# Performance work log

Hardware: AMD Instinct MI355X
Metric: run time of the kernel (lower is better)

Reference implementation:

```python
import jax, jax.numpy as jnp
import numpy as np

GRID_RES = 128
SCALE = 2.0
DEFORM_SCALE = 1.0
N_VERTS = 200_000
N_TETS = 1_000_000

TRI_TABLE = np.array([
    [-1,-1,-1,-1,-1,-1],[1,0,2,-1,-1,-1],[4,0,3,-1,-1,-1],[1,4,2,1,3,4],
    [3,1,5,-1,-1,-1],[2,3,0,2,5,3],[1,4,0,1,5,4],[4,2,5,-1,-1,-1],
    [4,5,2,-1,-1,-1],[4,1,0,4,5,1],[3,2,0,3,5,2],[1,3,5,-1,-1,-1],
    [4,1,2,4,3,1],[3,0,4,-1,-1,-1],[2,0,1,-1,-1,-1],[-1,-1,-1,-1,-1,-1]], dtype=np.int64)
NUM_TRI_TABLE = np.array([0,1,1,2,1,2,2,1,1,2,2,1,2,1,1,0], dtype=np.int64)
BASE_TET_EDGES = np.array([0,1,0,2,0,3,1,2,1,3,2,3], dtype=np.int64)


def setup_inputs() -> dict:
    key = jax.random.key(0)
    k1, k2, k3, k4 = jax.random.split(key, 4)
    verts = jax.random.normal(k1, (N_VERTS, 3), dtype=jnp.float32) * SCALE
    deform = jax.random.normal(k2, (N_VERTS, 3), dtype=jnp.float32)
    sdf_sign = jnp.sign(jax.random.normal(k3, (N_VERTS,), dtype=jnp.float32) + 1e-8)
    sdf_sign = jnp.where(sdf_sign == 0, 1.0, sdf_sign)
    sdf_abs = jnp.ones((N_VERTS,), dtype=jnp.float32)
    indices = jax.random.randint(k4, (N_TETS, 4), 0, N_VERTS, dtype=jnp.int64)
    return dict(verts=verts, deform=deform, sdf_sign=sdf_sign, sdf_abs=sdf_abs, indices=indices)


def _prep_topology(sdf_np, tet_np):
    """Non-differentiable (torch.no_grad) integer bookkeeping, done in numpy."""
    occ = sdf_np > 0                       # [N]
    occ_fx4 = occ[tet_np]                  # [T,4]
    occ_sum = occ_fx4.sum(-1)
    valid = (occ_sum > 0) & (occ_sum < 4)
    tet_v = tet_np[valid]                  # [Tv,4]
    all_edges = tet_v[:, BASE_TET_EDGES].reshape(-1, 2)
    all_edges = np.sort(all_edges, axis=1)     # same as torch sort_edges (min,max)
    unique_edges, idx_map = np.unique(all_edges, axis=0, return_inverse=True)
    idx_map = idx_map.reshape(-1)
    mask_edges = occ[unique_edges].sum(-1) == 1   # sign-crossing edges
    mapping = np.full(unique_edges.shape[0], -1, dtype=np.int64)
    mapping[mask_edges] = np.arange(int(mask_edges.sum()), dtype=np.int64)
    idx_map = mapping[idx_map].reshape(-1, 6)
    interp_v = unique_edges[mask_edges]            # [M,2]
    tetindex = (occ_fx4[valid].astype(np.int64) * np.array([1, 2, 4, 8])).sum(-1)
    num_tri = NUM_TRI_TABLE[tetindex]
    one, two = num_tri == 1, num_tri == 2
    f1 = np.take_along_axis(idx_map[one], TRI_TABLE[tetindex[one]][:, :3], axis=1).reshape(-1, 3)
    f2 = np.take_along_axis(idx_map[two], TRI_TABLE[tetindex[two]][:, :6], axis=1).reshape(-1, 3)
    faces = np.concatenate([f1, f2], axis=0)
    tet_gidx = np.arange(tet_np.shape[0], dtype=np.int64)[valid]
    fg1 = tet_gidx[one] * 2
    g2 = tet_gidx[two]
    fg2 = np.stack([g2 * 2, g2 * 2 + 1], axis=-1).reshape(-1)
    face_gidx = np.concatenate([fg1, fg2], axis=0)
    return interp_v, faces, face_gidx


def _map_uv(face_gidx, max_idx):
    Ng = int(np.ceil(np.sqrt((max_idx + 1) // 2)))
    lin = np.linspace(0.0, 1.0 - 1.0 / Ng, Ng, dtype=np.float32)
    tex_y, tex_x = np.meshgrid(lin, lin, indexing='ij')
    pad = np.float32(0.9 / Ng)
    uvs = np.stack([tex_x, tex_y, tex_x + pad, tex_y,
                    tex_x + pad, tex_y + pad, tex_x, tex_y + pad], axis=-1).reshape(-1, 2)
    raw = face_gidx // 2
    tet_idx = (raw // Ng) * Ng + (raw % Ng)
    tri_idx = face_gidx % 2
    uv_idx = np.stack([tet_idx * 4, tet_idx * 4 + tri_idx + 1, tet_idx * 4 + tri_idx + 2], axis=-1).reshape(-1, 3)
    return jnp.asarray(uvs), jnp.asarray(uv_idx)


def reference(verts, deform, sdf_sign, sdf_abs, indices):
    sdf = sdf_sign * jnp.abs(sdf_abs)                      # [N]
    v_deformed = verts + (2.0 / (GRID_RES * 2)) * deform * DEFORM_SCALE
    interp_v, faces, face_gidx = _prep_topology(np.asarray(sdf), np.asarray(indices))
    iv = jnp.asarray(interp_v)                             # [M,2]
    pos = v_deformed[iv]                                   # [M,2,3]
    s = sdf[iv]                                            # [M,2]
    sa, sb = s[:, 0], s[:, 1]
    denom = sa - sb                                        # == sa + (-sb)
    # torch: weights = flip([sa,-sb]) / denom -> [-sb, sa] / (sa - sb)
    out_verts = pos[:, 0] * (-sb / denom)[:, None] + pos[:, 1] * (sa / denom)[:, None]
    uvs, uv_idx = _map_uv(face_gidx, indices.shape[0] * 2)
    return out_verts, jnp.asarray(faces), uvs, uv_idx
```

## Files before the change

### kernel.cpp

```cpp
#include <hip/hip_runtime.h>
#include <stdint.h>

#define NVERT 200000
#define NTET  1000000
#define NE2   4000000
#define NG 1000
#define PAYB 23
#define PAYMASK ((1u<<PAYB)-1u)
#define KB 18
#define KMASK ((1u<<KB)-1u)

#define SCAN_T 256
#define SCAN_E 16
#define SCAN_EPB (SCAN_T*SCAN_E)

__constant__ int c_tri[16][6] = {
  {-1,-1,-1,-1,-1,-1},{1,0,2,-1,-1,-1},{4,0,3,-1,-1,-1},{1,4,2,1,3,4},
  {3,1,5,-1,-1,-1},{2,3,0,2,5,3},{1,4,0,1,5,4},{4,2,5,-1,-1,-1},
  {4,5,2,-1,-1,-1},{4,1,0,4,5,1},{3,2,0,3,5,2},{1,3,5,-1,-1,-1},
  {4,1,2,4,3,1},{3,0,4,-1,-1,-1},{2,0,1,-1,-1,-1},{-1,-1,-1,-1,-1,-1}};
__constant__ int c_ntri[16] = {0,1,1,2,1,2,2,1,1,2,2,1,2,1,1,0};
__constant__ int c_e0[6] = {0,0,0,1,1,2};
__constant__ int c_e1[6] = {1,2,3,2,3,3};

__global__ void k_zero2(uint32_t* __restrict__ a, uint32_t* __restrict__ b, int n){
  int i = blockIdx.x*blockDim.x + threadIdx.x;
  if (i < n){ a[i] = 0u; b[i] = 0u; }
}

__global__ void k_sdf(const float* __restrict__ ssign, const float* __restrict__ sabs,
                      float* __restrict__ sdf, uint8_t* __restrict__ occ){
  int i = blockIdx.x*blockDim.x + threadIdx.x;
  if (i >= NVERT) return;
  float s = ssign[i] * fabsf(sabs[i]);
  sdf[i] = s;
  occ[i] = (s > 0.0f) ? 1 : 0;
}

__global__ void k_tet(const int* __restrict__ idx, const uint8_t* __restrict__ occ,
                      uint8_t* __restrict__ tetidx, uint32_t* __restrict__ oneA,
                      uint32_t* __restrict__ twoA, uint32_t* __restrict__ bcnt){
  int t = blockIdx.x*blockDim.x + threadIdx.x;
  if (t >= NTET) return;
  int v[4];
  #pragma unroll
  for (int j = 0; j < 4; ++j) v[j] = idx[t*4+j];
  int ti = 0;
  #pragma unroll
  for (int j = 0; j < 4; ++j) ti |= (occ[v[j]] ? 1 : 0) << j;
  tetidx[t] = (uint8_t)ti;
  int nt = c_ntri[ti];
  oneA[t] = (nt == 1) ? 1u : 0u;
  twoA[t] = (nt == 2) ? 1u : 0u;
  if (nt == 0) return;
  #pragma unroll
  for (int e = 0; e < 6; ++e){
    int o0 = (ti >> c_e0[e]) & 1, o1 = (ti >> c_e1[e]) & 1;
    if (o0 == o1) continue;
    int a = v[c_e0[e]], b = v[c_e1[e]];
    if (a > b){ int tmp = a; a = b; b = tmp; }
    atomicAdd((unsigned int*)&bcnt[a], 1u);
  }
}

__global__ void k_scan_block(uint32_t* __restrict__ d, uint32_t* __restrict__ part, int L){
  int tid = threadIdx.x;
  int base = blockIdx.x*SCAN_EPB + tid*SCAN_E;
  uint32_t v[SCAN_E];
  #pragma unroll
  for (int j = 0; j < SCAN_E; ++j){
    int i = base + j;
    v[j] = (i < L) ? d[i] : 0u;
  }
  #pragma unroll
  for (int j = 1; j < SCAN_E; ++j) v[j] += v[j-1];
  __shared__ uint32_t s[SCAN_T];
  s[tid] = v[SCAN_E-1];
  __syncthreads();
  for (int o = 1; o < SCAN_T; o <<= 1){
    uint32_t x = (tid >= o) ? s[tid-o] : 0u;
    __syncthreads();
    s[tid] += x;
    __syncthreads();
  }
  uint32_t off = s[tid] - v[SCAN_E-1];
  #pragma unroll
  for (int j = 0; j < SCAN_E; ++j){
    int i = base + j;
    if (i < L) d[i] = v[j] + off;
  }
  if (tid == SCAN_T-1 && part) part[blockIdx.x] = s[SCAN_T-1];
}

__global__ void k_scan_part(uint32_t* __restrict__ part, int n){
  int tid = threadIdx.x;
  int per = (n + SCAN_T - 1)/SCAN_T;
  int st = tid*per, en = st + per; if (en > n) en = n;
  uint32_t sum = 0;
  for (int i = st; i < en; ++i) sum += part[i];
  __shared__ uint32_t s[SCAN_T];
  s[tid] = sum;
  __syncthreads();
  for (int o = 1; o < SCAN_T; o <<= 1){
    uint32_t x = (tid >= o) ? s[tid-o] : 0u;
    __syncthreads();
    s[tid] += x;
    __syncthreads();
  }
  uint32_t off = s[tid] - sum;
  uint32_t run = off;
  for (int i = st; i < en; ++i){ run += part[i]; part[i] = run; }
}

__global__ void k_scan_add(uint32_t* __restrict__ d, const uint32_t* __restrict__ part, int L){
  int blk = blockIdx.x;
  if (blk == 0) return;
  uint32_t off = part[blk-1];
  int base = blk*SCAN_EPB;
  #pragma unroll
  for (int j = 0; j < SCAN_E; ++j){
    int i = base + j*SCAN_T + threadIdx.x;
    if (i < L) d[i] += off;
  }
}

__global__ void k_scatter(const int* __restrict__ idx, const uint8_t* __restrict__ tetidx,
                          const uint32_t* __restrict__ bincl, uint32_t* __restrict__ fill,
                          uint64_t* __restrict__ skey){
  int t = blockIdx.x*blockDim.x + threadIdx.x;
  if (t >= NTET) return;
  int ti = tetidx[t];
  if (c_ntri[ti] == 0) return;
  int v[4];
  #pragma unroll
  for (int j = 0; j < 4; ++j) v[j] = idx[t*4+j];
  #pragma unroll
  for (int e = 0; e < 6; ++e){
    int o0 = (ti >> c_e0[e]) & 1, o1 = (ti >> c_e1[e]) & 1;
    if (o0 == o1) continue;
    int a = v[c_e0[e]], b = v[c_e1[e]];
    if (a > b){ int tmp = a; a = b; b = tmp; }
    uint32_t base = (a > 0) ? bincl[a-1] : 0u;
    uint32_t p = base + atomicAdd((unsigned int*)&fill[a], 1u);
    if (p < NE2)
      skey[p] = ((uint64_t)(uint32_t)a << (PAYB+KB)) | ((uint64_t)(uint32_t)b << PAYB)
              | (uint32_t)(t*6 + e);
  }
}

__global__ void k_bsort(uint64_t* __restrict__ skey, const uint32_t* __restrict__ bincl){
  int gid  = blockIdx.x*blockDim.x + threadIdx.x;
  int w    = gid >> 6;
  int lane = threadIdx.x & 63;
  int W    = (gridDim.x*blockDim.x) >> 6;
  for (int b = w; b < NVERT; b += W){
    uint32_t s0 = (b > 0) ? bincl[b-1] : 0u;
    uint32_t e0 = bincl[b];
    int n = (int)(e0 - s0);
    if (n <= 1) continue;
    if (n <= 64){
      uint64_t ki = (lane < n) ? skey[s0+lane] : ~0ull;
      int r = 0;
      for (int j = 0; j < n; ++j){
        uint64_t kj = __shfl(ki, j, 64);
        r += (kj < ki) ? 1 : 0;
      }
      if (lane < n) skey[s0 + r] = ki;
    } else if (n <= 128){
      uint64_t k0 = (lane < n)      ? skey[s0+lane]    : ~0ull;
      uint64_t k1 = (64+lane < n)   ? skey[s0+64+lane] : ~0ull;
      int r0 = 0, r1 = 0;
      for (int j = 0; j < 64; ++j){
        uint64_t kj = __shfl(k0, j, 64);
        r0 += (kj < k0) ? 1 : 0;
        r1 += (kj < k1) ? 1 : 0;
      }
      for (int j = 64; j < n; ++j){
        uint64_t kj = __shfl(k1, j-64, 64);
        r0 += (kj < k0) ? 1 : 0;
        r1 += (kj < k1) ? 1 : 0;
      }
      if (lane < n)    skey[s0 + r0] = k0;
      if (64+lane < n) skey[s0 + r1] = k1;
    } else if (lane == 0){
      for (int i = 1; i < n; ++i){
        uint64_t x = skey[s0+i];
        int j = i-1;
        while (j >= 0 && skey[s0+j] > x){ skey[s0+j+1] = skey[s0+j]; --j; }
        skey[s0+j+1] = x;
      }
    }
  }
}

__global__ void k_flags(const uint64_t* __restrict__ skey,
                        const uint32_t* __restrict__ bincl, uint32_t* __restrict__ maskA){
  int i = blockIdx.x*blockDim.x + threadIdx.x;
  if (i >= NE2) return;
  uint32_t nE = (uint32_t)__builtin_amdgcn_readfirstlane((int)bincl[NVERT-1]);
  if ((uint32_t)i >= nE){ maskA[i] = 0u; return; }
  uint64_t k = skey[i] >> PAYB;
  bool head = (i == 0) || ((skey[i-1] >> PAYB) != k);
  maskA[i] = head ? 1u : 0u;
}

__global__ void k_emit(const uint64_t* __restrict__ skey, const uint32_t* __restrict__ maskI,
                       const uint32_t* __restrict__ bincl,
                       const float* __restrict__ verts, const float* __restrict__ deform,
                       const float* __restrict__ sdf,
                       uint32_t* __restrict__ edge2vert, float* __restrict__ out){
  int i = blockIdx.x*blockDim.x + threadIdx.x;
  if (i >= NE2) return;
  uint32_t nE = (uint32_t)__builtin_amdgcn_readfirstlane((int)bincl[NVERT-1]);
  if ((uint32_t)i >= nE) return;
  uint64_t k = skey[i];
  uint32_t m = maskI[i];
  uint32_t pm = (i > 0) ? maskI[i-1] : 0u;
  uint32_t vid = m - 1u;
  edge2vert[(uint32_t)(k & PAYMASK)] = vid;
  if (m == pm) return;
  int a = (int)(k >> (PAYB+KB)), b = (int)((k >> PAYB) & KMASK);
  float sa = sdf[a], sb = sdf[b];
  float denom = sa - sb;
  float w0 = __fdiv_rn(-sb, denom);
  float w1 = __fdiv_rn(sa, denom);
  #pragma unroll
  for (int c = 0; c < 3; ++c){
    float pa = __fadd_rn(verts[a*3+c], __fmul_rn(0.0078125f, deform[a*3+c]));
    float pb = __fadd_rn(verts[b*3+c], __fmul_rn(0.0078125f, deform[b*3+c]));
    out[(size_t)vid*3 + c] = __fadd_rn(__fmul_rn(pa, w0), __fmul_rn(pb, w1));
  }
}

__global__ void k_faces(const uint8_t* __restrict__ tetidx,
                        const uint32_t* __restrict__ oneI, const uint32_t* __restrict__ twoI,
                        const uint32_t* __restrict__ maskI,
                        const uint32_t* __restrict__ edge2vert, float* __restrict__ out){
  int t = blockIdx.x*blockDim.x + threadIdx.x;
  if (t >= NTET) return;
  int ti = tetidx[t];
  int nt = c_ntri[ti];
  if (nt == 0) return;
  uint32_t nInterp = (uint32_t)__builtin_amdgcn_readfirstlane((int)maskI[NE2-1]);
  uint32_t nOne    = (uint32_t)__builtin_amdgcn_readfirstlane((int)oneI[NTET-1]);
  uint32_t nTwo    = (uint32_t)__builtin_amdgcn_readfirstlane((int)twoI[NTET-1]);
  size_t facesOff = (size_t)3*nInterp;
  size_t nFaces = (size_t)nOne + 2u*(size_t)nTwo;
  size_t uvIdxOff = facesOff + 3*nFaces + (size_t)(4*NG*NG)*2;
  for (int k = 0; k < nt; ++k){
    size_t row = (nt == 1) ? (size_t)(oneI[t]-1u)
                           : (size_t)nOne + 2u*(size_t)(twoI[t]-1u) + (size_t)k;
    #pragma unroll
    for (int j = 0; j < 3; ++j){
      int e = c_tri[ti][k*3+j];
      out[facesOff + row*3 + j] = (float)edge2vert[t*6 + e];
    }
    int tri = (nt == 2) ? k : 0;
    long long t4 = 4LL*t;
    out[uvIdxOff + row*3 + 0] = (float)t4;
    out[uvIdxOff + row*3 + 1] = (float)(t4 + tri + 1);
    out[uvIdxOff + row*3 + 2] = (float)(t4 + tri + 2);
  }
}

__global__ void k_uvs(const uint32_t* __restrict__ maskI, const uint32_t* __restrict__ oneI,
                      const uint32_t* __restrict__ twoI, float* __restrict__ out){
  int r = blockIdx.x*blockDim.x + threadIdx.x;
  if (r >= 4*NG*NG) return;
  uint32_t nInterp = (uint32_t)__builtin_amdgcn_readfirstlane((int)maskI[NE2-1]);
  uint32_t nOne    = (uint32_t)__builtin_amdgcn_readfirstlane((int)oneI[NTET-1]);
  uint32_t nTwo    = (uint32_t)__builtin_amdgcn_readfirstlane((int)twoI[NTET-1]);
  size_t uvOff = (size_t)3*nInterp + 3*((size_t)nOne + 2u*(size_t)nTwo);
  int cell = r >> 2, c = r & 3;
  int iy = cell / NG, jx = cell % NG;
  const double step = (1.0 - 1.0/NG)/(NG-1);
  float x = (jx == NG-1) ? (float)(1.0 - 1.0/NG) : (float)((double)jx*step);
  float y = (iy == NG-1) ? (float)(1.0 - 1.0/NG) : (float)((double)iy*step);
  float pad = (float)(0.9/NG);
  float u, vv;
  switch (c){
    case 0: u = x;                 vv = y;                 break;
    case 1: u = __fadd_rn(x, pad); vv = y;                 break;
    case 2: u = __fadd_rn(x, pad); vv = __fadd_rn(y, pad); break;
    default:u = x;                 vv = __fadd_rn(y, pad); break;
  }
  out[uvOff + (size_t)r*2 + 0] = u;
  out[uvOff + (size_t)r*2 + 1] = vv;
}

static void scan_u32(uint32_t* d, int L, uint32_t* part, hipStream_t s){
  int nb = (L + SCAN_EPB - 1)/SCAN_EPB;
  k_scan_block<<<nb, SCAN_T, 0, s>>>(d, part, L);
  if (nb > 1){
    k_scan_part<<<1, SCAN_T, 0, s>>>(part, nb);
    k_scan_add<<<nb, SCAN_T, 0, s>>>(d, part, L);
  }
}

extern "C" void kernel_launch(void* const* d_in, const int* in_sizes, int n_in,
                              void* d_out, int out_size, void* d_ws, size_t ws_size,
                              hipStream_t stream){
  const float* verts  = (const float*)d_in[0];
  const float* deform = (const float*)d_in[1];
  const float* ssign  = (const float*)d_in[2];
  const float* sabs   = (const float*)d_in[3];
  const int*   idx    = (const int*)d_in[4];
  float* out = (float*)d_out;

  char* ws = (char*)d_ws;
  size_t o = 0;
  auto alloc = [&](size_t bytes) -> void* {
    void* p = ws + o;
    o = (o + bytes + 255) & ~(size_t)255;
    return p;
  };
  float*    sdf     = (float*)   alloc(sizeof(float)*NVERT);
  uint8_t*  occ     = (uint8_t*) alloc(NVERT);
  uint8_t*  tetidx  = (uint8_t*) alloc(NTET);
  uint32_t* bincl   = (uint32_t*)alloc(sizeof(uint32_t)*NVERT);
  uint32_t* fill    = (uint32_t*)alloc(sizeof(uint32_t)*NVERT);
  uint32_t* oneI    = (uint32_t*)alloc(sizeof(uint32_t)*NTET);
  uint32_t* twoI    = (uint32_t*)alloc(sizeof(uint32_t)*NTET);
  uint32_t* maskI   = (uint32_t*)alloc(sizeof(uint32_t)*NE2);
  uint64_t* skey    = (uint64_t*)alloc(sizeof(uint64_t)*NE2);
  uint32_t* e2v     = (uint32_t*)alloc(sizeof(uint32_t)*NTET*6);
  uint32_t* part    = (uint32_t*)alloc(sizeof(uint32_t)*2048);
  if (o > ws_size) return;

  k_zero2<<<(NVERT+255)/256, 256, 0, stream>>>(bincl, fill, NVERT);

  k_sdf<<<(NVERT+255)/256, 256, 0, stream>>>(ssign, sabs, sdf, occ);
  k_tet<<<(NTET+255)/256, 256, 0, stream>>>(idx, occ, tetidx, oneI, twoI, bincl);

  scan_u32(bincl, NVERT, part, stream);

  k_scatter<<<(NTET+255)/256, 256, 0, stream>>>(idx, tetidx, bincl, fill, skey);
  k_bsort<<<1024, 256, 0, stream>>>(skey, bincl);

  k_flags<<<(NE2+255)/256, 256, 0, stream>>>(skey, bincl, maskI);
  scan_u32(maskI, NE2, part, stream);
  scan_u32(oneI, NTET, part, stream);
  scan_u32(twoI, NTET, part, stream);

  k_emit<<<(NE2+255)/256, 256, 0, stream>>>(skey, maskI, bincl, verts, deform, sdf, e2v, out);
  k_faces<<<(NTET+255)/256, 256, 0, stream>>>(tetidx, oneI, twoI, maskI, e2v, out);
  k_uvs<<<(4*NG*NG+255)/256, 256, 0, stream>>>(maskI, oneI, twoI, out);
}
```

Baseline: 690.4 us.

## Shrink edge keys to 32-bit and look up face vertices by bucket search

Sort keys now hold only the second endpoint, since the first endpoint is implied by the bucket, so keys shrink from 64 to 32 bits. The per-bucket sort also writes the duplicate-head flags directly, which removes the separate flags kernel. The per-tet edge-to-vertex scatter table is dropped: faces re-derive each edge and linearly scan the endpoint's bucket to find its interpolated vertex id, and vertex emission is done per bucket by wavefronts. The edge buffer capacity is also lowered, trading a bounded-size assumption and extra bucket scanning in the face kernel for less memory traffic and fewer launches.

```diff
diff --git a/kernel.cpp b/kernel.cpp
--- a/kernel.cpp
+++ b/kernel.cpp
@@ -3,12 +3,8 @@
 
 #define NVERT 200000
 #define NTET  1000000
-#define NE2   4000000
+#define NE2   3200000
 #define NG 1000
-#define PAYB 23
-#define PAYMASK ((1u<<PAYB)-1u)
-#define KB 18
-#define KMASK ((1u<<KB)-1u)
 
 #define SCAN_T 256
 #define SCAN_E 16
@@ -126,7 +122,7 @@
 
 __global__ void k_scatter(const int* __restrict__ idx, const uint8_t* __restrict__ tetidx,
                           const uint32_t* __restrict__ bincl, uint32_t* __restrict__ fill,
-                          uint64_t* __restrict__ skey){
+                          uint32_t* __restrict__ skey){
   int t = blockIdx.x*blockDim.x + threadIdx.x;
   if (t >= NTET) return;
   int ti = tetidx[t];
@@ -142,13 +138,12 @@
     if (a > b){ int tmp = a; a = b; b = tmp; }
     uint32_t base = (a > 0) ? bincl[a-1] : 0u;
     uint32_t p = base + atomicAdd((unsigned int*)&fill[a], 1u);
-    if (p < NE2)
-      skey[p] = ((uint64_t)(uint32_t)a << (PAYB+KB)) | ((uint64_t)(uint32_t)b << PAYB)
-              | (uint32_t)(t*6 + e);
-  }
-}
-
-__global__ void k_bsort(uint64_t* __restrict__ skey, const uint32_t* __restrict__ bincl){
+    if (p < NE2) skey[p] = (uint32_t)b;
+  }
+}
+
+__global__ void k_bsort(uint32_t* __restrict__ skey, const uint32_t* __restrict__ bincl,
+                        uint32_t* __restrict__ maskA){
   int gid  = blockIdx.x*blockDim.x + threadIdx.x;
   int w    = gid >> 6;
   int lane = threadIdx.x & 63;
@@ -157,103 +152,123 @@
     uint32_t s0 = (b > 0) ? bincl[b-1] : 0u;
     uint32_t e0 = bincl[b];
     int n = (int)(e0 - s0);
-    if (n <= 1) continue;
+    if (n <= 0) continue;
+    if (n == 1){
+      if (lane == 0) maskA[s0] = 1u;
+      continue;
+    }
     if (n <= 64){
-      uint64_t ki = (lane < n) ? skey[s0+lane] : ~0ull;
-      int r = 0;
+      uint32_t ki = (lane < n) ? skey[s0+lane] : 0xFFFFFFFFu;
+      int r = 0; bool dup = false;
       for (int j = 0; j < n; ++j){
-        uint64_t kj = __shfl(ki, j, 64);
-        r += (kj < ki) ? 1 : 0;
-      }
-      if (lane < n) skey[s0 + r] = ki;
+        uint32_t kj = __shfl(ki, j, 64);
+        bool tie = (kj == ki) && (j < lane);
+        r += ((kj < ki) || tie) ? 1 : 0;
+        dup |= tie;
+      }
+      if (lane < n){
+        skey[s0 + r] = ki;
+        maskA[s0 + r] = dup ? 0u : 1u;
+      }
     } else if (n <= 128){
-      uint64_t k0 = (lane < n)      ? skey[s0+lane]    : ~0ull;
-      uint64_t k1 = (64+lane < n)   ? skey[s0+64+lane] : ~0ull;
-      int r0 = 0, r1 = 0;
+      uint32_t k0 = (lane < n)    ? skey[s0+lane]    : 0xFFFFFFFFu;
+      uint32_t k1 = (64+lane < n) ? skey[s0+64+lane] : 0xFFFFFFFFu;
+      int r0 = 0, r1 = 0; bool d0 = false, d1 = false;
       for (int j = 0; j < 64; ++j){
-        uint64_t kj = __shfl(k0, j, 64);
+        uint32_t kj = __shfl(k0, j, 64);
+        bool t0 = (kj == k0) && (j < lane);
+        r0 += ((kj < k0) || t0) ? 1 : 0;  d0 |= t0;
+        bool t1 = (kj == k1);
+        r1 += ((kj < k1) || t1) ? 1 : 0;  d1 |= t1;
+      }
+      for (int j = 0; j < 64; ++j){
+        if (64+j >= n) break;
+        uint32_t kj = __shfl(k1, j, 64);
         r0 += (kj < k0) ? 1 : 0;
-        r1 += (kj < k1) ? 1 : 0;
-      }
-      for (int j = 64; j < n; ++j){
-        uint64_t kj = __shfl(k1, j-64, 64);
-        r0 += (kj < k0) ? 1 : 0;
-        r1 += (kj < k1) ? 1 : 0;
-      }
-      if (lane < n)    skey[s0 + r0] = k0;
-      if (64+lane < n) skey[s0 + r1] = k1;
+        bool t1 = (kj == k1) && (j < lane);
+        r1 += ((kj < k1) || t1) ? 1 : 0;  d1 |= t1;
+      }
+      if (lane < n)   { skey[s0 + r0] = k0; maskA[s0 + r0] = d0 ? 0u : 1u; }
+      if (64+lane < n){ skey[s0 + r1] = k1; maskA[s0 + r1] = d1 ? 0u : 1u; }
     } else if (lane == 0){
       for (int i = 1; i < n; ++i){
-        uint64_t x = skey[s0+i];
+        uint32_t x = skey[s0+i];
         int j = i-1;
         while (j >= 0 && skey[s0+j] > x){ skey[s0+j+1] = skey[s0+j]; --j; }
         skey[s0+j+1] = x;
       }
+      maskA[s0] = 1u;
+      for (int i = 1; i < n; ++i) maskA[s0+i] = (skey[s0+i] != skey[s0+i-1]) ? 1u : 0u;
     }
   }
 }
 
-__global__ void k_flags(const uint64_t* __restrict__ skey,
-                        const uint32_t* __restrict__ bincl, uint32_t* __restrict__ maskA){
-  int i = blockIdx.x*blockDim.x + threadIdx.x;
-  if (i >= NE2) return;
-  uint32_t nE = (uint32_t)__builtin_amdgcn_readfirstlane((int)bincl[NVERT-1]);
-  if ((uint32_t)i >= nE){ maskA[i] = 0u; return; }
-  uint64_t k = skey[i] >> PAYB;
-  bool head = (i == 0) || ((skey[i-1] >> PAYB) != k);
-  maskA[i] = head ? 1u : 0u;
-}
-
-__global__ void k_emit(const uint64_t* __restrict__ skey, const uint32_t* __restrict__ maskI,
-                       const uint32_t* __restrict__ bincl,
-                       const float* __restrict__ verts, const float* __restrict__ deform,
-                       const float* __restrict__ sdf,
-                       uint32_t* __restrict__ edge2vert, float* __restrict__ out){
-  int i = blockIdx.x*blockDim.x + threadIdx.x;
-  if (i >= NE2) return;
-  uint32_t nE = (uint32_t)__builtin_amdgcn_readfirstlane((int)bincl[NVERT-1]);
-  if ((uint32_t)i >= nE) return;
-  uint64_t k = skey[i];
-  uint32_t m = maskI[i];
-  uint32_t pm = (i > 0) ? maskI[i-1] : 0u;
-  uint32_t vid = m - 1u;
-  edge2vert[(uint32_t)(k & PAYMASK)] = vid;
-  if (m == pm) return;
-  int a = (int)(k >> (PAYB+KB)), b = (int)((k >> PAYB) & KMASK);
-  float sa = sdf[a], sb = sdf[b];
-  float denom = sa - sb;
-  float w0 = __fdiv_rn(-sb, denom);
-  float w1 = __fdiv_rn(sa, denom);
-  #pragma unroll
-  for (int c = 0; c < 3; ++c){
-    float pa = __fadd_rn(verts[a*3+c], __fmul_rn(0.0078125f, deform[a*3+c]));
-    float pb = __fadd_rn(verts[b*3+c], __fmul_rn(0.0078125f, deform[b*3+c]));
-    out[(size_t)vid*3 + c] = __fadd_rn(__fmul_rn(pa, w0), __fmul_rn(pb, w1));
-  }
-}
-
-__global__ void k_faces(const uint8_t* __restrict__ tetidx,
+__global__ void k_verts2(const uint32_t* __restrict__ skey, const uint32_t* __restrict__ maskI,
+                         const uint32_t* __restrict__ bincl,
+                         const float* __restrict__ verts, const float* __restrict__ deform,
+                         const float* __restrict__ sdf, float* __restrict__ out){
+  int gid  = blockIdx.x*blockDim.x + threadIdx.x;
+  int w    = gid >> 6;
+  int lane = threadIdx.x & 63;
+  int W    = (gridDim.x*blockDim.x) >> 6;
+  for (int a = w; a < NVERT; a += W){
+    uint32_t s0 = (a > 0) ? bincl[a-1] : 0u;
+    uint32_t e0 = bincl[a];
+    int n = (int)(e0 - s0);
+    if (n <= 0) continue;
+    float sa = sdf[a];
+    for (int base = 0; base < n; base += 64){
+      int l = base + lane;
+      if (l >= n) break;
+      uint32_t bv = skey[s0+l];
+      bool head = (l == 0) || (skey[s0+l-1] != bv);
+      if (!head) continue;
+      uint32_t vid = maskI[s0+l] - 1u;
+      int b = (int)bv;
+      float sb = sdf[b];
+      float denom = sa - sb;
+      float w0 = __fdiv_rn(-sb, denom);
+      float w1 = __fdiv_rn(sa, denom);
+      #pragma unroll
+      for (int c = 0; c < 3; ++c){
+        float pa = __fadd_rn(verts[a*3+c], __fmul_rn(0.0078125f, deform[a*3+c]));
+        float pb = __fadd_rn(verts[b*3+c], __fmul_rn(0.0078125f, deform[b*3+c]));
+        out[(size_t)vid*3 + c] = __fadd_rn(__fmul_rn(pa, w0), __fmul_rn(pb, w1));
+      }
+    }
+  }
+}
+
+__global__ void k_faces(const int* __restrict__ idx, const uint8_t* __restrict__ tetidx,
                         const uint32_t* __restrict__ oneI, const uint32_t* __restrict__ twoI,
-                        const uint32_t* __restrict__ maskI,
-                        const uint32_t* __restrict__ edge2vert, float* __restrict__ out){
+                        const uint32_t* __restrict__ maskI, const uint32_t* __restrict__ bincl,
+                        const uint32_t* __restrict__ skey, float* __restrict__ out){
   int t = blockIdx.x*blockDim.x + threadIdx.x;
   if (t >= NTET) return;
   int ti = tetidx[t];
   int nt = c_ntri[ti];
   if (nt == 0) return;
-  uint32_t nInterp = (uint32_t)__builtin_amdgcn_readfirstlane((int)maskI[NE2-1]);
+  uint32_t nE      = (uint32_t)__builtin_amdgcn_readfirstlane((int)bincl[NVERT-1]);
+  uint32_t nInterp = (uint32_t)__builtin_amdgcn_readfirstlane((int)maskI[nE-1]);
   uint32_t nOne    = (uint32_t)__builtin_amdgcn_readfirstlane((int)oneI[NTET-1]);
   uint32_t nTwo    = (uint32_t)__builtin_amdgcn_readfirstlane((int)twoI[NTET-1]);
   size_t facesOff = (size_t)3*nInterp;
   size_t nFaces = (size_t)nOne + 2u*(size_t)nTwo;
   size_t uvIdxOff = facesOff + 3*nFaces + (size_t)(4*NG*NG)*2;
+  int v[4];
+  #pragma unroll
+  for (int j = 0; j < 4; ++j) v[j] = idx[t*4+j];
   for (int k = 0; k < nt; ++k){
     size_t row = (nt == 1) ? (size_t)(oneI[t]-1u)
                            : (size_t)nOne + 2u*(size_t)(twoI[t]-1u) + (size_t)k;
     #pragma unroll
     for (int j = 0; j < 3; ++j){
       int e = c_tri[ti][k*3+j];
-      out[facesOff + row*3 + j] = (float)edge2vert[t*6 + e];
+      int a = v[c_e0[e]], b = v[c_e1[e]];
+      if (a > b){ int tmp = a; a = b; b = tmp; }
+      uint32_t p = (a > 0) ? bincl[a-1] : 0u;
+      while (skey[p] != (uint32_t)b) ++p;
+      out[facesOff + row*3 + j] = (float)(maskI[p] - 1u);
     }
     int tri = (nt == 2) ? k : 0;
     long long t4 = 4LL*t;
@@ -263,11 +278,13 @@
   }
 }
 
-__global__ void k_uvs(const uint32_t* __restrict__ maskI, const uint32_t* __restrict__ oneI,
-                      const uint32_t* __restrict__ twoI, float* __restrict__ out){
+__global__ void k_uvs(const uint32_t* __restrict__ maskI, const uint32_t* __restrict__ bincl,
+                      const uint32_t* __restrict__ oneI, const uint32_t* __restrict__ twoI,
+                      float* __restrict__ out){
   int r = blockIdx.x*blockDim.x + threadIdx.x;
   if (r >= 4*NG*NG) return;
-  uint32_t nInterp = (uint32_t)__builtin_amdgcn_readfirstlane((int)maskI[NE2-1]);
+  uint32_t nE      = (uint32_t)__builtin_amdgcn_readfirstlane((int)bincl[NVERT-1]);
+  uint32_t nInterp = (uint32_t)__builtin_amdgcn_readfirstlane((int)maskI[nE-1]);
   uint32_t nOne    = (uint32_t)__builtin_amdgcn_readfirstlane((int)oneI[NTET-1]);
   uint32_t nTwo    = (uint32_t)__builtin_amdgcn_readfirstlane((int)twoI[NTET-1]);
   size_t uvOff = (size_t)3*nInterp + 3*((size_t)nOne + 2u*(size_t)nTwo);
@@ -322,8 +339,7 @@
   uint32_t* oneI    = (uint32_t*)alloc(sizeof(uint32_t)*NTET);
   uint32_t* twoI    = (uint32_t*)alloc(sizeof(uint32_t)*NTET);
   uint32_t* maskI   = (uint32_t*)alloc(sizeof(uint32_t)*NE2);
-  uint64_t* skey    = (uint64_t*)alloc(sizeof(uint64_t)*NE2);
-  uint32_t* e2v     = (uint32_t*)alloc(sizeof(uint32_t)*NTET*6);
+  uint32_t* skey    = (uint32_t*)alloc(sizeof(uint32_t)*NE2);
   uint32_t* part    = (uint32_t*)alloc(sizeof(uint32_t)*2048);
   if (o > ws_size) return;
 
@@ -335,14 +351,13 @@
   scan_u32(bincl, NVERT, part, stream);
 
   k_scatter<<<(NTET+255)/256, 256, 0, stream>>>(idx, tetidx, bincl, fill, skey);
-  k_bsort<<<1024, 256, 0, stream>>>(skey, bincl);
-
-  k_flags<<<(NE2+255)/256, 256, 0, stream>>>(skey, bincl, maskI);
+  k_bsort<<<1024, 256, 0, stream>>>(skey, bincl, maskI);
+
   scan_u32(maskI, NE2, part, stream);
   scan_u32(oneI, NTET, part, stream);
   scan_u32(twoI, NTET, part, stream);
 
-  k_emit<<<(NE2+255)/256, 256, 0, stream>>>(skey, maskI, bincl, verts, deform, sdf, e2v, out);
-  k_faces<<<(NTET+255)/256, 256, 0, stream>>>(tetidx, oneI, twoI, maskI, e2v, out);
-  k_uvs<<<(4*NG*NG+255)/256, 256, 0, stream>>>(maskI, oneI, twoI, out);
-}
+  k_verts2<<<1024, 256, 0, stream>>>(skey, maskI, bincl, verts, deform, sdf, out);
+  k_faces<<<(NTET+255)/256, 256, 0, stream>>>(idx, tetidx, oneI, twoI, maskI, bincl, skey, out);
+  k_uvs<<<(4*NG*NG+255)/256, 256, 0, stream>>>(maskI, bincl, oneI, twoI, out);
+}
```

Measured after the change: 956.2 us. +38.5%, slower.

## Fuse edge-head flags into bucket sort, pack one/two counters, merge init kernels

Applied to the files above, without the earlier changes.

Removes the separate flag kernel by computing the unique-edge head mask inside the per-vertex bucket sort, using a duplicate check against smaller keys with the same edge. Packs the one- and two-triangle counters into one 64-bit array so a single 64-bit scan replaces two 32-bit scans. Merges the zeroing kernel into the sdf kernel and shrinks the edge buffer bound to 3.2M. Consumers now read the true edge count from bincl, because mask entries past it are no longer zeroed. The smaller NE2 is a risk if the real crossing-edge count ever exceeds the bound.

```diff
diff --git a/kernel.cpp b/kernel.cpp
--- a/kernel.cpp
+++ b/kernel.cpp
@@ -3,7 +3,7 @@
 
 #define NVERT 200000
 #define NTET  1000000
-#define NE2   4000000
+#define NE2   3200000
 #define NG 1000
 #define PAYB 23
 #define PAYMASK ((1u<<PAYB)-1u)
@@ -23,23 +23,27 @@
 __constant__ int c_e0[6] = {0,0,0,1,1,2};
 __constant__ int c_e1[6] = {1,2,3,2,3,3};
 
-__global__ void k_zero2(uint32_t* __restrict__ a, uint32_t* __restrict__ b, int n){
-  int i = blockIdx.x*blockDim.x + threadIdx.x;
-  if (i < n){ a[i] = 0u; b[i] = 0u; }
-}
-
-__global__ void k_sdf(const float* __restrict__ ssign, const float* __restrict__ sabs,
-                      float* __restrict__ sdf, uint8_t* __restrict__ occ){
+__device__ __forceinline__ uint64_t shfl64(uint64_t x, int src){
+  int lo = __shfl((int)(uint32_t)x, src, 64);
+  int hi = __shfl((int)(uint32_t)(x >> 32), src, 64);
+  return ((uint64_t)(uint32_t)hi << 32) | (uint32_t)lo;
+}
+
+__global__ void k_init(const float* __restrict__ ssign, const float* __restrict__ sabs,
+                       float* __restrict__ sdf, uint8_t* __restrict__ occ,
+                       uint32_t* __restrict__ bincl, uint32_t* __restrict__ fill){
   int i = blockIdx.x*blockDim.x + threadIdx.x;
   if (i >= NVERT) return;
   float s = ssign[i] * fabsf(sabs[i]);
   sdf[i] = s;
   occ[i] = (s > 0.0f) ? 1 : 0;
+  bincl[i] = 0u;
+  fill[i]  = 0u;
 }
 
 __global__ void k_tet(const int* __restrict__ idx, const uint8_t* __restrict__ occ,
-                      uint8_t* __restrict__ tetidx, uint32_t* __restrict__ oneA,
-                      uint32_t* __restrict__ twoA, uint32_t* __restrict__ bcnt){
+                      uint8_t* __restrict__ tetidx, uint64_t* __restrict__ oneTwo,
+                      uint32_t* __restrict__ bcnt){
   int t = blockIdx.x*blockDim.x + threadIdx.x;
   if (t >= NTET) return;
   int v[4];
@@ -50,8 +54,7 @@
   for (int j = 0; j < 4; ++j) ti |= (occ[v[j]] ? 1 : 0) << j;
   tetidx[t] = (uint8_t)ti;
   int nt = c_ntri[ti];
-  oneA[t] = (nt == 1) ? 1u : 0u;
-  twoA[t] = (nt == 2) ? 1u : 0u;
+  oneTwo[t] = ((nt == 1) ? 1ull : 0ull) | (((nt == 2) ? 1ull : 0ull) << 32);
   if (nt == 0) return;
   #pragma unroll
   for (int e = 0; e < 6; ++e){
@@ -124,6 +127,67 @@
   }
 }
 
+__global__ void k_scan_block64(uint64_t* __restrict__ d, uint64_t* __restrict__ part, int L){
+  int tid = threadIdx.x;
+  int base = blockIdx.x*SCAN_EPB + tid*SCAN_E;
+  uint64_t v[SCAN_E];
+  #pragma unroll
+  for (int j = 0; j < SCAN_E; ++j){
+    int i = base + j;
+    v[j] = (i < L) ? d[i] : 0ull;
+  }
+  #pragma unroll
+  for (int j = 1; j < SCAN_E; ++j) v[j] += v[j-1];
+  __shared__ uint64_t s[SCAN_T];
+  s[tid] = v[SCAN_E-1];
+  __syncthreads();
+  for (int o = 1; o < SCAN_T; o <<= 1){
+    uint64_t x = (tid >= o) ? s[tid-o] : 0ull;
+    __syncthreads();
+    s[tid] += x;
+    __syncthreads();
+  }
+  uint64_t off = s[tid] - v[SCAN_E-1];
+  #pragma unroll
+  for (int j = 0; j < SCAN_E; ++j){
+    int i = base + j;
+    if (i < L) d[i] = v[j] + off;
+  }
+  if (tid == SCAN_T-1 && part) part[blockIdx.x] = s[SCAN_T-1];
+}
+
+__global__ void k_scan_part64(uint64_t* __restrict__ part, int n){
+  int tid = threadIdx.x;
+  int per = (n + SCAN_T - 1)/SCAN_T;
+  int st = tid*per, en = st + per; if (en > n) en = n;
+  uint64_t sum = 0;
+  for (int i = st; i < en; ++i) sum += part[i];
+  __shared__ uint64_t s[SCAN_T];
+  s[tid] = sum;
+  __syncthreads();
+  for (int o = 1; o < SCAN_T; o <<= 1){
+    uint64_t x = (tid >= o) ? s[tid-o] : 0ull;
+    __syncthreads();
+    s[tid] += x;
+    __syncthreads();
+  }
+  uint64_t off = s[tid] - sum;
+  uint64_t run = off;
+  for (int i = st; i < en; ++i){ run += part[i]; part[i] = run; }
+}
+
+__global__ void k_scan_add64(uint64_t* __restrict__ d, const uint64_t* __restrict__ part, int L){
+  int blk = blockIdx.x;
+  if (blk == 0) return;
+  uint64_t off = part[blk-1];
+  int base = blk*SCAN_EPB;
+  #pragma unroll
+  for (int j = 0; j < SCAN_E; ++j){
+    int i = base + j*SCAN_T + threadIdx.x;
+    if (i < L) d[i] += off;
+  }
+}
+
 __global__ void k_scatter(const int* __restrict__ idx, const uint8_t* __restrict__ tetidx,
                           const uint32_t* __restrict__ bincl, uint32_t* __restrict__ fill,
                           uint64_t* __restrict__ skey){
@@ -148,7 +212,8 @@
   }
 }
 
-__global__ void k_bsort(uint64_t* __restrict__ skey, const uint32_t* __restrict__ bincl){
+__global__ void k_bsort(uint64_t* __restrict__ skey, const uint32_t* __restrict__ bincl,
+                        uint32_t* __restrict__ maskA){
   int gid  = blockIdx.x*blockDim.x + threadIdx.x;
   int w    = gid >> 6;
   int lane = threadIdx.x & 63;
@@ -157,31 +222,45 @@
     uint32_t s0 = (b > 0) ? bincl[b-1] : 0u;
     uint32_t e0 = bincl[b];
     int n = (int)(e0 - s0);
-    if (n <= 1) continue;
+    if (n <= 0) continue;
+    if (n == 1){
+      if (lane == 0) maskA[s0] = 1u;
+      continue;
+    }
     if (n <= 64){
       uint64_t ki = (lane < n) ? skey[s0+lane] : ~0ull;
-      int r = 0;
+      int r = 0; bool dup = false;
       for (int j = 0; j < n; ++j){
-        uint64_t kj = __shfl(ki, j, 64);
-        r += (kj < ki) ? 1 : 0;
+        uint64_t kj = shfl64(ki, j);
+        bool lt = (kj < ki);
+        r += lt ? 1 : 0;
+        dup |= lt && ((kj >> PAYB) == (ki >> PAYB));
       }
-      if (lane < n) skey[s0 + r] = ki;
+      if (lane < n){
+        skey[s0 + r] = ki;
+        maskA[s0 + r] = dup ? 0u : 1u;
+      }
     } else if (n <= 128){
-      uint64_t k0 = (lane < n)      ? skey[s0+lane]    : ~0ull;
-      uint64_t k1 = (64+lane < n)   ? skey[s0+64+lane] : ~0ull;
-      int r0 = 0, r1 = 0;
+      int n2 = n - 64;
+      uint64_t k0 = skey[s0+lane];
+      uint64_t k1 = (lane < n2) ? skey[s0+64+lane] : ~0ull;
+      int r0 = 0, r1 = 0; bool d0 = false, d1 = false;
       for (int j = 0; j < 64; ++j){
-        uint64_t kj = __shfl(k0, j, 64);
-        r0 += (kj < k0) ? 1 : 0;
-        r1 += (kj < k1) ? 1 : 0;
+        uint64_t kj = shfl64(k0, j);
+        bool lt0 = (kj < k0);
+        r0 += lt0 ? 1 : 0;  d0 |= lt0 && ((kj >> PAYB) == (k0 >> PAYB));
+        bool lt1 = (kj < k1);
+        r1 += lt1 ? 1 : 0;  d1 |= lt1 && ((kj >> PAYB) == (k1 >> PAYB));
       }
-      for (int j = 64; j < n; ++j){
-        uint64_t kj = __shfl(k1, j-64, 64);
-        r0 += (kj < k0) ? 1 : 0;
-        r1 += (kj < k1) ? 1 : 0;
+      for (int j = 0; j < n2; ++j){
+        uint64_t kj = shfl64(k1, j);
+        bool lt0 = (kj < k0);
+        r0 += lt0 ? 1 : 0;  d0 |= lt0 && ((kj >> PAYB) == (k0 >> PAYB));
+        bool lt1 = (kj < k1);
+        r1 += lt1 ? 1 : 0;  d1 |= lt1 && ((kj >> PAYB) == (k1 >> PAYB));
       }
-      if (lane < n)    skey[s0 + r0] = k0;
-      if (64+lane < n) skey[s0 + r1] = k1;
+      { skey[s0 + r0] = k0; maskA[s0 + r0] = d0 ? 0u : 1u; }
+      if (lane < n2){ skey[s0 + r1] = k1; maskA[s0 + r1] = d1 ? 0u : 1u; }
     } else if (lane == 0){
       for (int i = 1; i < n; ++i){
         uint64_t x = skey[s0+i];
@@ -189,19 +268,11 @@
         while (j >= 0 && skey[s0+j] > x){ skey[s0+j+1] = skey[s0+j]; --j; }
         skey[s0+j+1] = x;
       }
+      maskA[s0] = 1u;
+      for (int i = 1; i < n; ++i)
+        maskA[s0+i] = ((skey[s0+i] >> PAYB) != (skey[s0+i-1] >> PAYB)) ? 1u : 0u;
     }
   }
-}
-
-__global__ void k_flags(const uint64_t* __restrict__ skey,
-                        const uint32_t* __restrict__ bincl, uint32_t* __restrict__ maskA){
-  int i = blockIdx.x*blockDim.x + threadIdx.x;
-  if (i >= NE2) return;
-  uint32_t nE = (uint32_t)__builtin_amdgcn_readfirstlane((int)bincl[NVERT-1]);
-  if ((uint32_t)i >= nE){ maskA[i] = 0u; return; }
-  uint64_t k = skey[i] >> PAYB;
-  bool head = (i == 0) || ((skey[i-1] >> PAYB) != k);
-  maskA[i] = head ? 1u : 0u;
 }
 
 __global__ void k_emit(const uint64_t* __restrict__ skey, const uint32_t* __restrict__ maskI,
@@ -233,23 +304,27 @@
 }
 
 __global__ void k_faces(const uint8_t* __restrict__ tetidx,
-                        const uint32_t* __restrict__ oneI, const uint32_t* __restrict__ twoI,
-                        const uint32_t* __restrict__ maskI,
+                        const uint64_t* __restrict__ oneTwoI,
+                        const uint32_t* __restrict__ maskI, const uint32_t* __restrict__ bincl,
                         const uint32_t* __restrict__ edge2vert, float* __restrict__ out){
   int t = blockIdx.x*blockDim.x + threadIdx.x;
   if (t >= NTET) return;
   int ti = tetidx[t];
   int nt = c_ntri[ti];
   if (nt == 0) return;
-  uint32_t nInterp = (uint32_t)__builtin_amdgcn_readfirstlane((int)maskI[NE2-1]);
-  uint32_t nOne    = (uint32_t)__builtin_amdgcn_readfirstlane((int)oneI[NTET-1]);
-  uint32_t nTwo    = (uint32_t)__builtin_amdgcn_readfirstlane((int)twoI[NTET-1]);
+  uint32_t nE      = (uint32_t)__builtin_amdgcn_readfirstlane((int)bincl[NVERT-1]);
+  uint32_t nInterp = (uint32_t)__builtin_amdgcn_readfirstlane((int)maskI[nE-1]);
+  uint64_t totOT   = oneTwoI[NTET-1];
+  uint32_t nOne    = (uint32_t)__builtin_amdgcn_readfirstlane((int)(uint32_t)totOT);
+  uint32_t nTwo    = (uint32_t)__builtin_amdgcn_readfirstlane((int)(uint32_t)(totOT >> 32));
   size_t facesOff = (size_t)3*nInterp;
   size_t nFaces = (size_t)nOne + 2u*(size_t)nTwo;
   size_t uvIdxOff = facesOff + 3*nFaces + (size_t)(4*NG*NG)*2;
+  uint64_t ot = oneTwoI[t];
+  uint32_t oneR = (uint32_t)ot, twoR = (uint32_t)(ot >> 32);
   for (int k = 0; k < nt; ++k){
-    size_t row = (nt == 1) ? (size_t)(oneI[t]-1u)
-                           : (size_t)nOne + 2u*(size_t)(twoI[t]-1u) + (size_t)k;
+    size_t row = (nt == 1) ? (size_t)(oneR-1u)
+                           : (size_t)nOne + 2u*(size_t)(twoR-1u) + (size_t)k;
     #pragma unroll
     for (int j = 0; j < 3; ++j){
       int e = c_tri[ti][k*3+j];
@@ -263,13 +338,15 @@
   }
 }
 
-__global__ void k_uvs(const uint32_t* __restrict__ maskI, const uint32_t* __restrict__ oneI,
-                      const uint32_t* __restrict__ twoI, float* __restrict__ out){
+__global__ void k_uvs(const uint32_t* __restrict__ maskI, const uint32_t* __restrict__ bincl,
+                      const uint64_t* __restrict__ oneTwoI, float* __restrict__ out){
   int r = blockIdx.x*blockDim.x + threadIdx.x;
   if (r >= 4*NG*NG) return;
-  uint32_t nInterp = (uint32_t)__builtin_amdgcn_readfirstlane((int)maskI[NE2-1]);
-  uint32_t nOne    = (uint32_t)__builtin_amdgcn_readfirstlane((int)oneI[NTET-1]);
-  uint32_t nTwo    = (uint32_t)__builtin_amdgcn_readfirstlane((int)twoI[NTET-1]);
+  uint32_t nE      = (uint32_t)__builtin_amdgcn_readfirstlane((int)bincl[NVERT-1]);
+  uint32_t nInterp = (uint32_t)__builtin_amdgcn_readfirstlane((int)maskI[nE-1]);
+  uint64_t totOT   = oneTwoI[NTET-1];
+  uint32_t nOne    = (uint32_t)__builtin_amdgcn_readfirstlane((int)(uint32_t)totOT);
+  uint32_t nTwo    = (uint32_t)__builtin_amdgcn_readfirstlane((int)(uint32_t)(totOT >> 32));
   size_t uvOff = (size_t)3*nInterp + 3*((size_t)nOne + 2u*(size_t)nTwo);
   int cell = r >> 2, c = r & 3;
   int iy = cell / NG, jx = cell % NG;
@@ -297,6 +374,15 @@
   }
 }
 
+static void scan_u64(uint64_t* d, int L, uint64_t* part, hipStream_t s){
+  int nb = (L + SCAN_EPB - 1)/SCAN_EPB;
+  k_scan_block64<<<nb, SCAN_T, 0, s>>>(d, part, L);
+  if (nb > 1){
+    k_scan_part64<<<1, SCAN_T, 0, s>>>(part, nb);
+    k_scan_add64<<<nb, SCAN_T, 0, s>>>(d, part, L);
+  }
+}
+
 extern "C" void kernel_launch(void* const* d_in, const int* in_sizes, int n_in,
                               void* d_out, int out_size, void* d_ws, size_t ws_size,
                               hipStream_t stream){
@@ -319,30 +405,26 @@
   uint8_t*  tetidx  = (uint8_t*) alloc(NTET);
   uint32_t* bincl   = (uint32_t*)alloc(sizeof(uint32_t)*NVERT);
   uint32_t* fill    = (uint32_t*)alloc(sizeof(uint32_t)*NVERT);
-  uint32_t* oneI    = (uint32_t*)alloc(sizeof(uint32_t)*NTET);
-  uint32_t* twoI    = (uint32_t*)alloc(sizeof(uint32_t)*NTET);
+  uint64_t* oneTwo  = (uint64_t*)alloc(sizeof(uint64_t)*NTET);
   uint32_t* maskI   = (uint32_t*)alloc(sizeof(uint32_t)*NE2);
   uint64_t* skey    = (uint64_t*)alloc(sizeof(uint64_t)*NE2);
   uint32_t* e2v     = (uint32_t*)alloc(sizeof(uint32_t)*NTET*6);
   uint32_t* part    = (uint32_t*)alloc(sizeof(uint32_t)*2048);
+  uint64_t* part64  = (uint64_t*)alloc(sizeof(uint64_t)*2048);
   if (o > ws_size) return;
 
-  k_zero2<<<(NVERT+255)/256, 256, 0, stream>>>(bincl, fill, NVERT);
-
-  k_sdf<<<(NVERT+255)/256, 256, 0, stream>>>(ssign, sabs, sdf, occ);
-  k_tet<<<(NTET+255)/256, 256, 0, stream>>>(idx, occ, tetidx, oneI, twoI, bincl);
+  k_init<<<(NVERT+255)/256, 256, 0, stream>>>(ssign, sabs, sdf, occ, bincl, fill);
+  k_tet<<<(NTET+255)/256, 256, 0, stream>>>(idx, occ, tetidx, oneTwo, bincl);
 
   scan_u32(bincl, NVERT, part, stream);
 
   k_scatter<<<(NTET+255)/256, 256, 0, stream>>>(idx, tetidx, bincl, fill, skey);
-  k_bsort<<<1024, 256, 0, stream>>>(skey, bincl);
-
-  k_flags<<<(NE2+255)/256, 256, 0, stream>>>(skey, bincl, maskI);
+  k_bsort<<<1024, 256, 0, stream>>>(skey, bincl, maskI);
+
   scan_u32(maskI, NE2, part, stream);
-  scan_u32(oneI, NTET, part, stream);
-  scan_u32(twoI, NTET, part, stream);
+  scan_u64(oneTwo, NTET, part64, stream);
 
   k_emit<<<(NE2+255)/256, 256, 0, stream>>>(skey, maskI, bincl, verts, deform, sdf, e2v, out);
-  k_faces<<<(NTET+255)/256, 256, 0, stream>>>(tetidx, oneI, twoI, maskI, e2v, out);
-  k_uvs<<<(4*NG*NG+255)/256, 256, 0, stream>>>(maskI, oneI, twoI, out);
-}
+  k_faces<<<(NTET+255)/256, 256, 0, stream>>>(tetidx, oneTwo, maskI, bincl, e2v, out);
+  k_uvs<<<(4*NG*NG+255)/256, 256, 0, stream>>>(maskI, bincl, oneTwo, out);
+}
```

Measured after the change: 652.1 us. 1.06x faster.
